# Kernel optimization log

Measured on AMD Instinct MI355X. Metric: run time of the kernel, lower is better.

The kernel has to match this reference:

```python
import jax, jax.numpy as jnp
import numpy as np

# Model dims (per init_kwargs)
DIM = 512
HEADS = 8
HD = DIM // HEADS          # head_dim = 64
NA = 32                    # num_agent_tokens
B, N = 4, 16384            # batch, flattened super-token count
SCALE = HD ** -0.5
NEG = -1e9                 # masked-softmax fill


def setup_inputs() -> dict:
    key = jax.random.key(0)
    ks = jax.random.split(key, 7)
    x = jax.random.normal(ks[0], (B, N, DIM), jnp.float32)
    mask = jax.random.randint(ks[1], (B, N), 0, 2).astype(jnp.int32)  # per-sample token validity mask
    agent_tokens = jax.random.normal(ks[2], (NA, DIM), jnp.float32) * 0.02  # trunc_normal(std=0.02) analog
    Wq = jax.random.normal(ks[3], (DIM, DIM), jnp.float32) / np.sqrt(DIM)
    Wk = jax.random.normal(ks[4], (DIM, DIM), jnp.float32) / np.sqrt(DIM)
    Wv = jax.random.normal(ks[5], (DIM, DIM), jnp.float32) / np.sqrt(DIM)
    Wproj = jax.random.normal(ks[6], (DIM, DIM), jnp.float32) / np.sqrt(DIM)
    return {"x": x, "mask": mask, "agent_tokens": agent_tokens,
            "Wq": Wq, "Wk": Wk, "Wv": Wv, "Wproj": Wproj}


def reference(x, mask, agent_tokens, Wq, Wk, Wv, Wproj):
    Bv, Nv, C = x.shape

    def heads(t):  # [B, N, C] -> [B, H, N, hd]
        return t.reshape(Bv, -1, HEADS, HD).transpose(0, 2, 1, 3)

    q = heads(x @ Wq)
    k = heads(x @ Wk)
    v = heads(x @ Wv)
    # agents: [Na, C] -> [B, H, Na, hd] (shared across batch)
    a = jnp.broadcast_to(
        agent_tokens.reshape(1, NA, HEADS, HD).transpose(0, 2, 1, 3),
        (Bv, HEADS, NA, HD))

    key_mask = (mask > 0)[:, None, None, :]              # [B,1,1,N]

    # Stage 1: agents attend to (masked) keys
    agent_attn = jnp.einsum('bhad,bhkd->bhak', a, k) * SCALE
    agent_attn = jnp.where(key_mask, agent_attn, NEG)
    agent_attn = jax.nn.softmax(agent_attn, axis=-1)
    agent_v = jnp.einsum('bhak,bhkd->bhad', agent_attn, v)  # [B,H,Na,hd]

    # Stage 2: queries attend to agents
    q_attn = jax.nn.softmax(jnp.einsum('bhqd,bhad->bhqa', q, a) * SCALE, axis=-1)
    out = jnp.einsum('bhqa,bhad->bhqd', q_attn, agent_v)     # [B,H,N,hd]

    out = out.transpose(0, 2, 1, 3).reshape(Bv, Nv, C) @ Wproj
    out = out * (mask > 0)[:, :, None].astype(out.dtype)    # zero invalid tokens
    return out
```

## Files before the change

### kernel.cpp

```cpp
#include <hip/hip_runtime.h>


typedef float  f32x4   __attribute__((ext_vector_type(4)));
typedef short  bf16x8  __attribute__((ext_vector_type(8)));
typedef unsigned short u16x4 __attribute__((ext_vector_type(4)));
typedef unsigned short u16x8 __attribute__((ext_vector_type(8)));

#define MFMA16(a, b, c) __builtin_amdgcn_mfma_f32_16x16x32_bf16((a), (b), (c), 0, 0, 0)

__device__ __forceinline__ unsigned short f2bf(float f) {
    unsigned u = __builtin_bit_cast(unsigned, f);
    u += 0x7FFFu + ((u >> 16) & 1u);
    return (unsigned short)(u >> 16);
}
__device__ __forceinline__ void gl2lds16(const void* g, void* l) {
    __builtin_amdgcn_global_load_lds(
        (const __attribute__((address_space(1))) unsigned int*)g,
        (__attribute__((address_space(3))) unsigned int*)l, 16, 0, 0);
}

__global__ __launch_bounds__(256) void k_cvt_x(const float* __restrict__ x,
                                               unsigned char* __restrict__ xt) {
    int v = blockIdx.x * 256 + threadIdx.x;
    int tile = v >> 10;
    int q = v & 1023;
    int row = q >> 3, c = q & 7;
    int mt = tile >> 3, ks = tile & 7;
    const float* sp = x + ((size_t)(mt * 128 + row)) * 512 + ks * 64 + c * 8;
    float4 v0 = *(const float4*)sp;
    float4 v1 = *(const float4*)(sp + 4);
    u16x8 o;
    o[0] = f2bf(v0.x); o[1] = f2bf(v0.y); o[2] = f2bf(v0.z); o[3] = f2bf(v0.w);
    o[4] = f2bf(v1.x); o[5] = f2bf(v1.y); o[6] = f2bf(v1.z); o[7] = f2bf(v1.w);
    *(u16x8*)(xt + (size_t)tile * 16384 + row * 128 + ((c ^ (row & 7)) << 4)) = o;
}

__global__ __launch_bounds__(256) void k_w_t_p(const float* __restrict__ Wp,
                                               unsigned short* __restrict__ Wpt) {
    __shared__ float t[32][33];
    const int k0 = blockIdx.y * 32, n0 = blockIdx.x * 32;
#pragma unroll
    for (int j = 0; j < 4; ++j) {
        int i = threadIdx.x + 256 * j;
        int ky = i >> 5, nx = i & 31;
        t[ky][nx] = Wp[(size_t)(k0 + ky) * 512 + n0 + nx];
    }
    __syncthreads();
#pragma unroll
    for (int j = 0; j < 4; ++j) {
        int i = threadIdx.x + 256 * j;
        int ny = i >> 5, kx = i & 31;
        Wpt[(size_t)(n0 + ny) * 512 + k0 + kx] = f2bf(t[kx][ny]);
    }
}

__global__ __launch_bounds__(256) void k_w_tile(const float* __restrict__ Wv,
                                                unsigned char* __restrict__ wtl2) {
    const int ks = blockIdx.x, nt = blockIdx.y;
    unsigned char* dst = wtl2 + ((size_t)(nt * 8 + ks)) * 16384;
    const int row = threadIdx.x & 63;
#pragma unroll
    for (int cc = 0; cc < 2; ++cc) {
        int c = (threadIdx.x >> 6) + cc * 4;
        u16x8 o;
#pragma unroll
        for (int j = 0; j < 8; ++j)
            o[j] = f2bf(Wv[(size_t)(ks * 64 + c * 8 + j) * 512 + nt * 64 + row]);
        *(u16x8*)(dst + row * 128 + ((c ^ (row & 7)) << 4)) = o;
    }
}

__global__ __launch_bounds__(256) void k_akw(const float* __restrict__ at,
                                             const float* __restrict__ Wk,
                                             const float* __restrict__ Wq,
                                             unsigned char* __restrict__ wtl2) {
    const int ks = blockIdx.x, h = blockIdx.y, which = blockIdx.z;
    const float* W = which ? Wq : Wk;
    const int row = threadIdx.x >> 3, c8 = threadIdx.x & 7;
    const float* ar = at + row * 512 + h * 64;
    float accv[8];
#pragma unroll
    for (int j = 0; j < 8; ++j) {
        const float* wr = W + (size_t)(ks * 64 + c8 * 8 + j) * 512 + h * 64;
        float s = 0.f;
#pragma unroll 8
        for (int d = 0; d < 64; ++d) s += ar[d] * wr[d];
        accv[j] = s;
    }
    u16x8 o;
#pragma unroll
    for (int j = 0; j < 8; ++j) o[j] = f2bf(accv[j]);
    *(u16x8*)(wtl2 + ((size_t)(h * 8 + ks)) * 16384 + 8192 + which * 4096 +
              row * 128 + ((c8 ^ (row & 7)) << 4)) = o;
}

__global__ __launch_bounds__(256) void k_qkvs(const unsigned char* __restrict__ xt,
                                              const unsigned char* __restrict__ wtl2,
                                              const int* __restrict__ mask,
                                              unsigned char* __restrict__ Qat,
                                              float* __restrict__ part_pv,
                                              float* __restrict__ part_ml) {
    __shared__ __align__(16) unsigned char S_[32768];
    unsigned char* As = S_;
    unsigned char* Bs = S_ + 16384;
    const int tid = threadIdx.x, l = tid & 63, wid = tid >> 6;
    const int g = l >> 4, lr = l & 15;
    const int dd = blockIdx.x;
    const int nt = (dd >> 3) & 7;
    const int mt = (dd & 7) + ((dd >> 6) << 3);
    const int m0 = mt * 128;
    const int b = mt >> 7, chunk = mt & 127, bh = b * 8 + nt;

    f32x4 acc[2][8] = {};

    for (int ks = 0; ks < 8; ++ks) {
        const size_t abase = ((size_t)(mt * 8 + ks)) * 16384;
        const size_t bbase = ((size_t)(nt * 8 + ks)) * 16384;
#pragma unroll
        for (int i = 0; i < 4; ++i)
            gl2lds16(xt + abase + i * 4096 + tid * 16, As + i * 4096 + tid * 16);
#pragma unroll
        for (int i = 0; i < 4; ++i)
            gl2lds16(wtl2 + bbase + i * 4096 + tid * 16, Bs + i * 4096 + tid * 16);
        __syncthreads();

        bf16x8 af[2][2];
#pragma unroll
        for (int mf = 0; mf < 2; ++mf) {
            int row = wid * 32 + mf * 16 + lr;
#pragma unroll
            for (int k2 = 0; k2 < 2; ++k2)
                af[mf][k2] = *(const bf16x8*)(As + row * 128 + (((k2 * 4 + g) ^ (row & 7)) << 4));
        }
#pragma unroll
        for (int k2 = 0; k2 < 2; ++k2) {
#pragma unroll
            for (int nf = 0; nf < 8; ++nf) {
                const int reg = (nf < 4) ? 0 : (8192 + ((nf >> 1) & 1) * 4096 + 0);
                const int sub = (nf < 4) ? nf : (nf & 1);
                const int regio = (nf < 4) ? 0 : (nf < 6 ? 8192 : 12288);
                int brow = sub * 16 + lr;
                bf16x8 bv = *(const bf16x8*)(Bs + regio + brow * 128 +
                                             (((k2 * 4 + g) ^ (brow & 7)) << 4));
                (void)reg;
#pragma unroll
                for (int mf = 0; mf < 2; ++mf)
                    acc[mf][nf] = MFMA16(af[mf][k2], bv, acc[mf][nf]);
            }
        }
        __syncthreads();
    }

    unsigned char* Psm_w = S_ + wid * 2048;
    unsigned char* Ev_w  = S_ + 8192 + wid * 4096;
    float* avsH = (float*)(S_ + 8192);
    float* redM = (float*)(S_ + 24576);
    float* redL = (float*)(S_ + 25088);

    {
        const size_t qbase = ((size_t)(mt * 4 + (nt >> 1))) * 16384;
        const int c80 = (nt & 1) * 4 + (lr >> 3);
#pragma unroll
        for (int mf = 0; mf < 2; ++mf) {
#pragma unroll
            for (int r = 0; r < 4; ++r) {
                float v0 = acc[mf][6][r] * 0.125f, v1 = acc[mf][7][r] * 0.125f;
                float m = fmaxf(v0, v1);
                m = fmaxf(m, __shfl_xor(m, 1));
                m = fmaxf(m, __shfl_xor(m, 2));
                m = fmaxf(m, __shfl_xor(m, 4));
                m = fmaxf(m, __shfl_xor(m, 8));
                float e0 = __expf(v0 - m), e1 = __expf(v1 - m);
                float s = e0 + e1;
                s += __shfl_xor(s, 1);
                s += __shfl_xor(s, 2);
                s += __shfl_xor(s, 4);
                s += __shfl_xor(s, 8);
                float inv = 1.0f / s;
                int row = wid * 32 + mf * 16 + g * 4 + r;
                size_t rb = qbase + row * 128 + (lr & 7) * 2;
                *(unsigned short*)(Qat + rb + ((c80 ^ (row & 7)) << 4)) = f2bf(e0 * inv);
                *(unsigned short*)(Qat + rb + (((c80 + 2) ^ (row & 7)) << 4)) = f2bf(e1 * inv);
            }
        }
    }

#pragma unroll
    for (int mf = 0; mf < 2; ++mf)
#pragma unroll
        for (int vf = 0; vf < 4; ++vf) {
            int d5 = vf * 16 + lr;
            u16x4 vv;
            vv[0] = f2bf(acc[mf][vf][0]); vv[1] = f2bf(acc[mf][vf][1]);
            vv[2] = f2bf(acc[mf][vf][2]); vv[3] = f2bf(acc[mf][vf][3]);
            *(u16x4*)(Ev_w + d5 * 64 + ((mf * 32 + g * 8) ^ ((d5 & 3) << 4))) = vv;
        }

    float sc2[2][2][4];
#pragma unroll
    for (int mf = 0; mf < 2; ++mf) {
        int4 mv = *(const int4*)(mask + m0 + wid * 32 + mf * 16 + g * 4);
        int mvr[4] = {mv.x, mv.y, mv.z, mv.w};
#pragma unroll
        for (int sf = 0; sf < 2; ++sf)
#pragma unroll
            for (int r = 0; r < 4; ++r)
                sc2[mf][sf][r] = (mvr[r] > 0) ? acc[mf][4 + sf][r] * 0.125f : -1.0e9f;
    }
    float mw[2];
#pragma unroll
    for (int sf = 0; sf < 2; ++sf) {
        float m = sc2[0][sf][0];
#pragma unroll
        for (int mf = 0; mf < 2; ++mf)
#pragma unroll
            for (int r = 0; r < 4; ++r) m = fmaxf(m, sc2[mf][sf][r]);
        m = fmaxf(m, __shfl_xor(m, 16));
        m = fmaxf(m, __shfl_xor(m, 32));
        mw[sf] = m;
    }
    if (g == 0) { redM[wid * 32 + lr] = mw[0]; redM[wid * 32 + 16 + lr] = mw[1]; }
    __syncthreads();
    float Mb[2];
#pragma unroll
    for (int sf = 0; sf < 2; ++sf) {
        int ag = sf * 16 + lr;
        Mb[sf] = fmaxf(fmaxf(redM[ag], redM[32 + ag]), fmaxf(redM[64 + ag], redM[96 + ag]));
    }
    float le[2] = {0.f, 0.f};
#pragma unroll
    for (int mf = 0; mf < 2; ++mf)
#pragma unroll
        for (int sf = 0; sf < 2; ++sf)
#pragma unroll
            for (int r = 0; r < 4; ++r) {
                float p = __expf(sc2[mf][sf][r] - Mb[sf]);
                le[sf] += p;
                int ag = sf * 16 + lr;
                int tk = mf * 16 + g * 4 + r;
                *(unsigned short*)(Psm_w + ag * 64 + ((2 * tk) ^ (((ag >> 2) & 3) << 4))) = f2bf(p);
            }
#pragma unroll
    for (int sf = 0; sf < 2; ++sf) {
        le[sf] += __shfl_xor(le[sf], 16);
        le[sf] += __shfl_xor(le[sf], 32);
    }
    if (g == 0) { redL[wid * 32 + lr] = le[0]; redL[wid * 32 + 16 + lr] = le[1]; }

    bf16x8 pa[2];
#pragma unroll
    for (int agf = 0; agf < 2; ++agf) {
        int ag = agf * 16 + lr;
        pa[agf] = *(const bf16x8*)(Psm_w + ag * 64 + ((g * 16) ^ (((ag >> 2) & 3) << 4)));
    }
    f32x4 pv[2][4] = {};
#pragma unroll
    for (int vf = 0; vf < 4; ++vf) {
        int d5 = vf * 16 + lr;
        bf16x8 bv = *(const bf16x8*)(Ev_w + d5 * 64 + ((g * 16) ^ ((d5 & 3) << 4)));
#pragma unroll
        for (int agf = 0; agf < 2; ++agf)
            pv[agf][vf] = MFMA16(pa[agf], bv, pv[agf][vf]);
    }

    float* pout = part_pv + ((size_t)bh * 128 + chunk) * 2048;
#pragma unroll
    for (int agf = 0; agf < 2; ++agf) {
#pragma unroll
        for (int vf = 0; vf < 4; ++vf)
#pragma unroll
            for (int r = 0; r < 4; ++r)
                avsH[wid * 1024 + (g * 4 + r) * 64 + vf * 16 + lr] = pv[agf][vf][r];
        __syncthreads();
#pragma unroll
        for (int j = 0; j < 4; ++j) {
            int idx = tid + 256 * j;
            pout[agf * 1024 + idx] = avsH[idx] + avsH[1024 + idx] +
                                     avsH[2048 + idx] + avsH[3072 + idx];
        }
        if (agf == 0) __syncthreads();
    }
    if (wid == 0 && g == 0) {
        size_t o = ((size_t)bh * 128 + chunk) * 64;
        float L0 = redL[lr] + redL[32 + lr] + redL[64 + lr] + redL[96 + lr];
        float L1 = redL[16 + lr] + redL[48 + lr] + redL[80 + lr] + redL[112 + lr];
        part_ml[o + lr * 2] = Mb[0];
        part_ml[o + lr * 2 + 1] = L0;
        part_ml[o + (16 + lr) * 2] = Mb[1];
        part_ml[o + (16 + lr) * 2 + 1] = L1;
    }
}

__global__ __launch_bounds__(256) void k_agent_comb(const float* __restrict__ part_pv,
                                                    const float* __restrict__ part_ml,
                                                    unsigned short* __restrict__ avbf) {
    __shared__ float scl[128][4];
    __shared__ float iLg[4], Mg[4];
    const int tid = threadIdx.x;
    const int ag0 = blockIdx.x * 4, bh = blockIdx.y;
    if (tid < 4) {
        int ag = ag0 + tid;
        const float* ml = part_ml + (size_t)bh * 8192 + ag * 2;
        float M = -3.0e38f;
#pragma unroll 4
        for (int c = 0; c < 128; ++c) M = fmaxf(M, ml[c * 64]);
        float L = 0.f;
#pragma unroll 4
        for (int c = 0; c < 128; ++c) L += __expf(ml[c * 64] - M) * ml[c * 64 + 1];
        Mg[tid] = M; iLg[tid] = 1.0f / L;
    }
    __syncthreads();
#pragma unroll
    for (int it = 0; it < 2; ++it) {
        int idx = tid + 256 * it;
        int c = idx >> 2, agl = idx & 3;
        scl[c][agl] = __expf(part_ml[(size_t)bh * 8192 + (size_t)c * 64 + (ag0 + agl) * 2] - Mg[agl]);
    }
    __syncthreads();
    const int agl = tid >> 6, d5 = tid & 63;
    const float* pv = part_pv + (size_t)bh * 128 * 2048 + (size_t)(ag0 + agl) * 64 + d5;
    float a = 0.f;
#pragma unroll 4
    for (int c = 0; c < 128; ++c) a += scl[c][agl] * pv[(size_t)c * 2048];
    avbf[(size_t)bh * 2048 + (size_t)(ag0 + agl) * 64 + d5] = f2bf(a * iLg[agl]);
}

__global__ __launch_bounds__(64) void k_avp(const unsigned short* __restrict__ avbf,
                                            const unsigned short* __restrict__ Wpt,
                                            unsigned char* __restrict__ AVPt) {
    const int l = threadIdx.x & 63;
    const int bh = blockIdx.x, b = bh >> 3, h = bh & 7;
    const int g = l >> 4, lr = l & 15;
    bf16x8 avf[2][2];
#pragma unroll
    for (int mf = 0; mf < 2; ++mf)
#pragma unroll
        for (int ks = 0; ks < 2; ++ks)
            avf[mf][ks] = *(const bf16x8*)(avbf + (size_t)bh * 2048 + (mf * 16 + lr) * 64 + ks * 32 + g * 8);
    const int kst = h >> 1;
#pragma unroll 4
    for (int nf = 0; nf < 32; ++nf) {
        int j = nf * 16 + lr;
        bf16x8 w0 = *(const bf16x8*)(Wpt + (size_t)j * 512 + h * 64 + g * 8);
        bf16x8 w1 = *(const bf16x8*)(Wpt + (size_t)j * 512 + h * 64 + 32 + g * 8);
        int jt = j >> 7, row = j & 127;
#pragma unroll
        for (int mf = 0; mf < 2; ++mf) {
            f32x4 z = {0.f, 0.f, 0.f, 0.f};
            f32x4 acc = MFMA16(avf[mf][0], w0, z);
            acc = MFMA16(avf[mf][1], w1, acc);
            u16x4 o;
            o[0] = f2bf(acc[0]); o[1] = f2bf(acc[1]); o[2] = f2bf(acc[2]); o[3] = f2bf(acc[3]);
            int c8 = (h & 1) * 4 + mf * 2 + (g >> 1);
            size_t byte = ((size_t)((b * 4 + jt) * 4 + kst)) * 16384 + row * 128 +
                          ((c8 ^ (row & 7)) << 4) + (g & 1) * 8;
            *(u16x4*)(AVPt + byte) = o;
        }
    }
}

__global__ __launch_bounds__(256) void k_out(const unsigned char* __restrict__ Qat,
                                             const unsigned char* __restrict__ AVPt,
                                             const int* __restrict__ mask,
                                             float* __restrict__ out) {
    __shared__ __align__(16) unsigned char As[16384];
    __shared__ __align__(16) unsigned char Bs[16384];
    const int tid = threadIdx.x, l = tid & 63, wid = tid >> 6;
    const int wm = wid >> 1, wn = wid & 1;
    const int g = l >> 4, lr = l & 15;
    const int d = blockIdx.x;
    const int nt = (d >> 3) & 3;
    const int mt = (d & 7) + ((d >> 5) << 3);
    const int m0 = mt * 128, j0 = nt * 128;
    const int b = m0 >> 14;
    f32x4 acc[4][4] = {};

    for (int ks = 0; ks < 4; ++ks) {
        const size_t abase = ((size_t)(mt * 4 + ks)) * 16384;
        const size_t bbase = ((size_t)((b * 4 + nt) * 4 + ks)) * 16384;
#pragma unroll
        for (int i = 0; i < 4; ++i) {
            gl2lds16(Qat + abase + i * 4096 + tid * 16, As + i * 4096 + tid * 16);
            gl2lds16(AVPt + bbase + i * 4096 + tid * 16, Bs + i * 4096 + tid * 16);
        }
        __syncthreads();
        bf16x8 af[4][2];
#pragma unroll
        for (int mf = 0; mf < 4; ++mf) {
            int row = wm * 64 + mf * 16 + lr;
#pragma unroll
            for (int k2 = 0; k2 < 2; ++k2)
                af[mf][k2] = *(const bf16x8*)(As + row * 128 + (((k2 * 4 + g) ^ (row & 7)) << 4));
        }
#pragma unroll
        for (int k2 = 0; k2 < 2; ++k2) {
#pragma unroll
            for (int nf = 0; nf < 4; ++nf) {
                int brow = wn * 64 + nf * 16 + lr;
                bf16x8 bv = *(const bf16x8*)(Bs + brow * 128 + (((k2 * 4 + g) ^ (brow & 7)) << 4));
#pragma unroll
                for (int mf = 0; mf < 4; ++mf)
                    acc[mf][nf] = MFMA16(af[mf][k2], bv, acc[mf][nf]);
            }
        }
        __syncthreads();
    }
#pragma unroll
    for (int mf = 0; mf < 4; ++mf) {
        int trow = m0 + wm * 64 + mf * 16 + g * 4;
#pragma unroll
        for (int r = 0; r < 4; ++r) {
            float mv = (mask[trow + r] > 0) ? 1.0f : 0.0f;
#pragma unroll
            for (int nf = 0; nf < 4; ++nf) {
                int j = j0 + wn * 64 + nf * 16 + lr;
                out[(size_t)(trow + r) * 512 + j] = acc[mf][nf][r] * mv;
            }
        }
    }
}

extern "C" void kernel_launch(void* const* d_in, const int* in_sizes, int n_in,
                              void* d_out, int out_size, void* d_ws, size_t ws_size,
                              hipStream_t stream) {
    const float* x  = (const float*)d_in[0];
    const int*  mk  = (const int*)d_in[1];
    const float* at = (const float*)d_in[2];
    const float* Wq = (const float*)d_in[3];
    const float* Wk = (const float*)d_in[4];
    const float* Wv = (const float*)d_in[5];
    const float* Wp = (const float*)d_in[6];
    float* out = (float*)d_out;
    char* ws = (char*)d_ws;

    unsigned char*  xt    = (unsigned char*)(ws);
    float* part_pv = (float*)(ws + ((size_t)64 << 20));
    float* part_ml = (float*)(ws + ((size_t)100 << 20));
    unsigned char*  Qat   = (unsigned char*)(ws + ((size_t)192 << 20));
    unsigned short* Wpt   = (unsigned short*)(ws + ((size_t)256 << 20));
    unsigned char*  wtl2  = (unsigned char*)(ws + ((size_t)258 << 20));
    unsigned short* avbf  = (unsigned short*)(ws + ((size_t)259 << 20) + (576 << 10));
    unsigned char*  AVPt  = (unsigned char*)(ws + ((size_t)260 << 20));

    k_cvt_x<<<16384, 256, 0, stream>>>(x, xt);
    k_w_t_p<<<dim3(16, 16), 256, 0, stream>>>(Wp, Wpt);
    k_w_tile<<<dim3(8, 8), 256, 0, stream>>>(Wv, wtl2);
    k_akw<<<dim3(8, 8, 2), 256, 0, stream>>>(at, Wk, Wq, wtl2);
    k_qkvs<<<4096, 256, 0, stream>>>(xt, wtl2, mk, Qat, part_pv, part_ml);
    k_agent_comb<<<dim3(8, 32), 256, 0, stream>>>(part_pv, part_ml, avbf);
    k_avp<<<32, 64, 0, stream>>>(avbf, Wpt, AVPt);
    k_out<<<2048, 256, 0, stream>>>(Qat, AVPt, mk, out);
}
```

Before: 244.5 us.

## Switch QKV GEMM warp tiling to 2x2 and split epilogue across warp roles

The fused QKV/score GEMM moves from four warps each owning 32 rows by all 128 columns to a 2x2 warp grid of 64 rows by 64 columns. This cuts the B-fragment LDS reads per warp and raises MFMA reuse per loaded fragment. The epilogue is also specialized: warps with wn=0 stage V into LDS while warps with wn=1 do the query softmax, the masked agent-score softmax and the P staging. The per-warp softmax reductions are replaced by a two-way reduction through LDS, at the cost of extra barriers, an unswizzled padded LDS layout and some warp imbalance in the epilogue.

```diff
diff --git a/kernel.cpp b/kernel.cpp
--- a/kernel.cpp
+++ b/kernel.cpp
@@ -105,13 +105,14 @@
     unsigned char* Bs = S_ + 16384;
     const int tid = threadIdx.x, l = tid & 63, wid = tid >> 6;
     const int g = l >> 4, lr = l & 15;
+    const int wm = wid >> 1, wn = wid & 1;
     const int dd = blockIdx.x;
     const int nt = (dd >> 3) & 7;
     const int mt = (dd & 7) + ((dd >> 6) << 3);
     const int m0 = mt * 128;
     const int b = mt >> 7, chunk = mt & 127, bh = b * 8 + nt;
 
-    f32x4 acc[2][8] = {};
+    f32x4 acc[4][4] = {};
 
     for (int ks = 0; ks < 8; ++ks) {
         const size_t abase = ((size_t)(mt * 8 + ks)) * 16384;
@@ -124,10 +125,10 @@
             gl2lds16(wtl2 + bbase + i * 4096 + tid * 16, Bs + i * 4096 + tid * 16);
         __syncthreads();
 
-        bf16x8 af[2][2];
-#pragma unroll
-        for (int mf = 0; mf < 2; ++mf) {
-            int row = wid * 32 + mf * 16 + lr;
+        bf16x8 af[4][2];
+#pragma unroll
+        for (int mf = 0; mf < 4; ++mf) {
+            int row = wm * 64 + mf * 16 + lr;
 #pragma unroll
             for (int k2 = 0; k2 < 2; ++k2)
                 af[mf][k2] = *(const bf16x8*)(As + row * 128 + (((k2 * 4 + g) ^ (row & 7)) << 4));
@@ -135,36 +136,48 @@
 #pragma unroll
         for (int k2 = 0; k2 < 2; ++k2) {
 #pragma unroll
-            for (int nf = 0; nf < 8; ++nf) {
-                const int reg = (nf < 4) ? 0 : (8192 + ((nf >> 1) & 1) * 4096 + 0);
-                const int sub = (nf < 4) ? nf : (nf & 1);
-                const int regio = (nf < 4) ? 0 : (nf < 6 ? 8192 : 12288);
-                int brow = sub * 16 + lr;
+            for (int nf = 0; nf < 4; ++nf) {
+                const int regio = wn ? (8192 + (nf >> 1) * 4096) : 0;
+                const int brow = (wn ? ((nf & 1) * 16) : (nf * 16)) + lr;
                 bf16x8 bv = *(const bf16x8*)(Bs + regio + brow * 128 +
                                              (((k2 * 4 + g) ^ (brow & 7)) << 4));
-                (void)reg;
-#pragma unroll
-                for (int mf = 0; mf < 2; ++mf)
+#pragma unroll
+                for (int mf = 0; mf < 4; ++mf)
                     acc[mf][nf] = MFMA16(af[mf][k2], bv, acc[mf][nf]);
             }
         }
         __syncthreads();
     }
 
-    unsigned char* Psm_w = S_ + wid * 2048;
-    unsigned char* Ev_w  = S_ + 8192 + wid * 4096;
-    float* avsH = (float*)(S_ + 8192);
-    float* redM = (float*)(S_ + 24576);
-    float* redL = (float*)(S_ + 25088);
-
-    {
+    unsigned char* Ph0 = S_;
+    unsigned char* Evh = S_ + 9216;
+    float* redM = (float*)(S_ + 27648);
+    float* redL = (float*)(S_ + 27904);
+    float* avsH = (float*)S_;
+
+    float sc2[4][2][4];
+    float Mb[2];
+
+    if (wn == 0) {
+        unsigned char* Ev = Evh + wm * 9216;
+#pragma unroll
+        for (int mf = 0; mf < 4; ++mf)
+#pragma unroll
+            for (int vf = 0; vf < 4; ++vf) {
+                int d5 = vf * 16 + lr;
+                u16x4 vv;
+                vv[0] = f2bf(acc[mf][vf][0]); vv[1] = f2bf(acc[mf][vf][1]);
+                vv[2] = f2bf(acc[mf][vf][2]); vv[3] = f2bf(acc[mf][vf][3]);
+                *(u16x4*)(Ev + d5 * 144 + mf * 32 + g * 8) = vv;
+            }
+    } else {
         const size_t qbase = ((size_t)(mt * 4 + (nt >> 1))) * 16384;
         const int c80 = (nt & 1) * 4 + (lr >> 3);
 #pragma unroll
-        for (int mf = 0; mf < 2; ++mf) {
+        for (int mf = 0; mf < 4; ++mf) {
 #pragma unroll
             for (int r = 0; r < 4; ++r) {
-                float v0 = acc[mf][6][r] * 0.125f, v1 = acc[mf][7][r] * 0.125f;
+                float v0 = acc[mf][2][r] * 0.125f, v1 = acc[mf][3][r] * 0.125f;
                 float m = fmaxf(v0, v1);
                 m = fmaxf(m, __shfl_xor(m, 1));
                 m = fmaxf(m, __shfl_xor(m, 2));
@@ -177,91 +190,85 @@
                 s += __shfl_xor(s, 4);
                 s += __shfl_xor(s, 8);
                 float inv = 1.0f / s;
-                int row = wid * 32 + mf * 16 + g * 4 + r;
+                int row = wm * 64 + mf * 16 + g * 4 + r;
                 size_t rb = qbase + row * 128 + (lr & 7) * 2;
                 *(unsigned short*)(Qat + rb + ((c80 ^ (row & 7)) << 4)) = f2bf(e0 * inv);
                 *(unsigned short*)(Qat + rb + (((c80 + 2) ^ (row & 7)) << 4)) = f2bf(e1 * inv);
             }
         }
-    }
-
-#pragma unroll
-    for (int mf = 0; mf < 2; ++mf)
-#pragma unroll
-        for (int vf = 0; vf < 4; ++vf) {
-            int d5 = vf * 16 + lr;
-            u16x4 vv;
-            vv[0] = f2bf(acc[mf][vf][0]); vv[1] = f2bf(acc[mf][vf][1]);
-            vv[2] = f2bf(acc[mf][vf][2]); vv[3] = f2bf(acc[mf][vf][3]);
-            *(u16x4*)(Ev_w + d5 * 64 + ((mf * 32 + g * 8) ^ ((d5 & 3) << 4))) = vv;
-        }
-
-    float sc2[2][2][4];
-#pragma unroll
-    for (int mf = 0; mf < 2; ++mf) {
-        int4 mv = *(const int4*)(mask + m0 + wid * 32 + mf * 16 + g * 4);
-        int mvr[4] = {mv.x, mv.y, mv.z, mv.w};
-#pragma unroll
-        for (int sf = 0; sf < 2; ++sf)
-#pragma unroll
-            for (int r = 0; r < 4; ++r)
-                sc2[mf][sf][r] = (mvr[r] > 0) ? acc[mf][4 + sf][r] * 0.125f : -1.0e9f;
-    }
-    float mw[2];
-#pragma unroll
-    for (int sf = 0; sf < 2; ++sf) {
-        float m = sc2[0][sf][0];
-#pragma unroll
-        for (int mf = 0; mf < 2; ++mf)
-#pragma unroll
-            for (int r = 0; r < 4; ++r) m = fmaxf(m, sc2[mf][sf][r]);
-        m = fmaxf(m, __shfl_xor(m, 16));
-        m = fmaxf(m, __shfl_xor(m, 32));
-        mw[sf] = m;
-    }
-    if (g == 0) { redM[wid * 32 + lr] = mw[0]; redM[wid * 32 + 16 + lr] = mw[1]; }
-    __syncthreads();
-    float Mb[2];
-#pragma unroll
-    for (int sf = 0; sf < 2; ++sf) {
-        int ag = sf * 16 + lr;
-        Mb[sf] = fmaxf(fmaxf(redM[ag], redM[32 + ag]), fmaxf(redM[64 + ag], redM[96 + ag]));
-    }
-    float le[2] = {0.f, 0.f};
-#pragma unroll
-    for (int mf = 0; mf < 2; ++mf)
-#pragma unroll
-        for (int sf = 0; sf < 2; ++sf)
-#pragma unroll
-            for (int r = 0; r < 4; ++r) {
-                float p = __expf(sc2[mf][sf][r] - Mb[sf]);
-                le[sf] += p;
+#pragma unroll
+        for (int mf = 0; mf < 4; ++mf) {
+            int4 mv = *(const int4*)(mask + m0 + wm * 64 + mf * 16 + g * 4);
+            int mvr[4] = {mv.x, mv.y, mv.z, mv.w};
+#pragma unroll
+            for (int sf = 0; sf < 2; ++sf)
+#pragma unroll
+                for (int r = 0; r < 4; ++r)
+                    sc2[mf][sf][r] = (mvr[r] > 0) ? acc[mf][sf][r] * 0.125f : -1.0e9f;
+        }
+#pragma unroll
+        for (int sf = 0; sf < 2; ++sf) {
+            float m = sc2[0][sf][0];
+#pragma unroll
+            for (int mf = 0; mf < 4; ++mf)
+#pragma unroll
+                for (int r = 0; r < 4; ++r) m = fmaxf(m, sc2[mf][sf][r]);
+            m = fmaxf(m, __shfl_xor(m, 16));
+            m = fmaxf(m, __shfl_xor(m, 32));
+            if (g == 0) redM[wm * 32 + sf * 16 + lr] = m;
+        }
+    }
+    __syncthreads();
+
+    if (wn == 1) {
+        float le[2] = {0.f, 0.f};
+#pragma unroll
+        for (int sf = 0; sf < 2; ++sf) {
+            int ag = sf * 16 + lr;
+            Mb[sf] = fmaxf(redM[ag], redM[32 + ag]);
+        }
+        unsigned char* Ph = Ph0 + wm * 4608;
+#pragma unroll
+        for (int mf = 0; mf < 4; ++mf)
+#pragma unroll
+            for (int sf = 0; sf < 2; ++sf) {
+                u16x4 p4;
+#pragma unroll
+                for (int r = 0; r < 4; ++r) {
+                    float p = __expf(sc2[mf][sf][r] - Mb[sf]);
+                    le[sf] += p;
+                    p4[r] = f2bf(p);
+                }
                 int ag = sf * 16 + lr;
-                int tk = mf * 16 + g * 4 + r;
-                *(unsigned short*)(Psm_w + ag * 64 + ((2 * tk) ^ (((ag >> 2) & 3) << 4))) = f2bf(p);
-            }
-#pragma unroll
-    for (int sf = 0; sf < 2; ++sf) {
-        le[sf] += __shfl_xor(le[sf], 16);
-        le[sf] += __shfl_xor(le[sf], 32);
-    }
-    if (g == 0) { redL[wid * 32 + lr] = le[0]; redL[wid * 32 + 16 + lr] = le[1]; }
-
+                *(u16x4*)(Ph + ag * 144 + mf * 32 + g * 8) = p4;
+            }
+#pragma unroll
+        for (int sf = 0; sf < 2; ++sf) {
+            le[sf] += __shfl_xor(le[sf], 16);
+            le[sf] += __shfl_xor(le[sf], 32);
+            if (g == 0) redL[wm * 32 + sf * 16 + lr] = le[sf];
+        }
+    }
+    __syncthreads();
+
+    const unsigned char* Ph = Ph0 + wm * 4608;
+    const unsigned char* Ev = Evh + wm * 9216;
     bf16x8 pa[2];
 #pragma unroll
     for (int agf = 0; agf < 2; ++agf) {
         int ag = agf * 16 + lr;
-        pa[agf] = *(const bf16x8*)(Psm_w + ag * 64 + ((g * 16) ^ (((ag >> 2) & 3) << 4)));
+        pa[agf] = *(const bf16x8*)(Ph + ag * 144 + wn * 64 + g * 16);
     }
     f32x4 pv[2][4] = {};
 #pragma unroll
     for (int vf = 0; vf < 4; ++vf) {
         int d5 = vf * 16 + lr;
-        bf16x8 bv = *(const bf16x8*)(Ev_w + d5 * 64 + ((g * 16) ^ ((d5 & 3) << 4)));
+        bf16x8 bv = *(const bf16x8*)(Ev + d5 * 144 + wn * 64 + g * 16);
 #pragma unroll
         for (int agf = 0; agf < 2; ++agf)
             pv[agf][vf] = MFMA16(pa[agf], bv, pv[agf][vf]);
     }
+    __syncthreads();
 
     float* pout = part_pv + ((size_t)bh * 128 + chunk) * 2048;
 #pragma unroll
@@ -280,10 +287,10 @@
         }
         if (agf == 0) __syncthreads();
     }
-    if (wid == 0 && g == 0) {
+    if (wid == 1 && g == 0) {
         size_t o = ((size_t)bh * 128 + chunk) * 64;
-        float L0 = redL[lr] + redL[32 + lr] + redL[64 + lr] + redL[96 + lr];
-        float L1 = redL[16 + lr] + redL[48 + lr] + redL[80 + lr] + redL[112 + lr];
+        float L0 = redL[lr] + redL[32 + lr];
+        float L1 = redL[16 + lr] + redL[48 + lr];
         part_ml[o + lr * 2] = Mb[0];
         part_ml[o + lr * 2 + 1] = L0;
         part_ml[o + (16 + lr) * 2] = Mb[1];
```

Measured after the change: 241.5 us. Within noise of the previous version (-1.2%).
